# Kernel optimization log

Hardware: AMD Instinct MI355X
Metric: run time of the kernel (lower is better)

The kernel has to match this reference:

```python
import jax, jax.numpy as jnp
import numpy as np

D_MODEL = 2048
D_INNER = 2048
N_QK = 32
N_V = 32
D_STATE = 64
D_CONV = 4
CHUNK = 128
CONV_DIM = D_INNER + 2 * N_QK * D_STATE  # 6144
IN_OUT = 2 * D_INNER + 2 * N_QK * D_STATE + N_V  # 8224


def setup_inputs() -> dict:
    key = jax.random.key(0)
    ks = jax.random.split(key, 6)
    u = jax.random.normal(ks[0], (2, 4096, D_MODEL), dtype=jnp.float32)
    W_in = jax.random.normal(ks[1], (IN_OUT, D_MODEL), dtype=jnp.float32) * 0.02
    conv_w = jax.random.normal(ks[2], (CONV_DIM, D_CONV), dtype=jnp.float32) * 0.2
    conv_b = jax.random.normal(ks[3], (CONV_DIM,), dtype=jnp.float32) * 0.02
    D = jnp.ones((N_V,), dtype=jnp.float32)
    z_bias = jnp.zeros((D_INNER,), dtype=jnp.float32)
    W_out = jax.random.normal(ks[4], (D_MODEL, D_INNER), dtype=jnp.float32) * 0.02
    return {"u": u, "W_in": W_in, "conv_w": conv_w, "conv_b": conv_b,
            "D": D, "z_bias": z_bias, "W_out": W_out}


def causal_depthwise_conv(x, w, b):
    # x: [B, L, C]; w: [C, K]; b: [C]. Torch Conv1d(groups=C, padding=K-1)[..., :L]
    B, L, C = x.shape
    K = w.shape[1]
    xp = jnp.pad(x, ((0, 0), (K - 1, 0), (0, 0)))
    y = b[None, None, :]
    for k in range(K):
        y = y + xp[:, k:k + L, :] * w[None, None, :, k]
    return y


def ssd_chunk_scan(x, dt, B, C, chunk):
    # Mamba2 SSD with A = -1 per head.
    # x: [b,l,h,p], dt: [b,l,h] (positive), B,C: [b,l,h,n]
    b, l, h, p = x.shape
    n = B.shape[-1]
    nc = l // chunk
    x = x.reshape(b, nc, chunk, h, p)
    dt = dt.reshape(b, nc, chunk, h)
    B = B.reshape(b, nc, chunk, h, n)
    C = C.reshape(b, nc, chunk, h, n)
    a = -dt                                  # A * dt
    cum = jnp.cumsum(a, axis=2)              # [b,nc,q,h]
    xdt = x * dt[..., None]                  # dt_t * x_t
    # ---- intra-chunk (causal, decay exp(cum_q - cum_k), q >= k) ----
    CB = jnp.einsum('bcqhn,bckhn->bchqk', C, B)
    cumT = jnp.swapaxes(cum, 2, 3)           # [b,nc,h,q]
    diff = cumT[..., :, None] - cumT[..., None, :]   # [b,nc,h,q,k]
    mask = jnp.tril(jnp.ones((chunk, chunk), dtype=bool))
    decay = jnp.exp(jnp.where(mask, diff, -jnp.inf))
    y_intra = jnp.einsum('bchqk,bckhp->bcqhp', CB * decay, xdt)
    # ---- per-chunk final states ----
    state_decay = jnp.exp(cum[:, :, -1:, :] - cum)   # [b,nc,q,h]
    states = jnp.einsum('bckhn,bckhp->bchpn', B * state_decay[..., None], xdt)
    chunk_decay = jnp.exp(cum[:, :, -1, :])          # [b,nc,h]
    # ---- inter-chunk recurrence ----
    def step(carry, inp):
        st, cd = inp  # st [b,h,p,n], cd [b,h]
        new = carry * cd[:, :, None, None] + st
        return new, carry  # emit the state *entering* this chunk
    init = jnp.zeros((b, h, p, n), dtype=x.dtype)
    _, prev = jax.lax.scan(step, init,
                           (jnp.moveaxis(states, 1, 0), jnp.moveaxis(chunk_decay, 1, 0)))
    prev = jnp.moveaxis(prev, 0, 1)                  # [b,nc,h,p,n]
    y_inter = jnp.einsum('bcqhn,bchpn->bcqhp', C * jnp.exp(cum)[..., None], prev)
    return (y_intra + y_inter).reshape(b, l, h, p)


def reference(u, W_in, conv_w, conv_b, D, z_bias, W_out):
    b, l, _ = u.shape  # l divisible by CHUNK (padded_len == l)
    xBCzA = jnp.einsum('bld,od->blo', u, W_in)
    xBC = xBCzA[..., :CONV_DIM]
    z = xBCzA[..., CONV_DIM:CONV_DIM + D_INNER]
    A_log = xBCzA[..., CONV_DIM + D_INNER:]
    xBC = causal_depthwise_conv(xBC, conv_w, conv_b)  # activation = identity
    x = xBC[..., :D_INNER]
    Bm = xBC[..., D_INNER:D_INNER + N_QK * D_STATE]
    Cm = xBC[..., D_INNER + N_QK * D_STATE:]
    x = x.reshape(b, l, N_V, D_INNER // N_V)
    Bm = Bm.reshape(b, l, N_QK, D_STATE)
    Cm = Cm.reshape(b, l, N_QK, D_STATE)
    dt = jax.nn.softplus(A_log)                       # [b,l,h]
    x_scan = x / dt[..., None]
    y = ssd_chunk_scan(x_scan, dt, Bm, Cm, CHUNK)
    y = y + D[None, None, :, None] * x                # Du uses undivided x
    y = y.reshape(b, l, D_INNER)
    out = jnp.einsum('bli,oi->blo', y * jax.nn.silu(z + z_bias), W_out)
    return out
```

## Files before the change

kernel.cpp:

```cpp
#include <hip/hip_runtime.h>
#include <math.h>

#define D_MODEL  2048
#define D_INNER  2048
#define N_QK     32
#define N_V      32
#define D_STATE  64
#define D_CONV   4
#define CHUNK    128
#define CONV_DIM 6144
#define IN_OUT   8224
#define BATCH    2
#define SEQ      4096
#define M_ROWS   (BATCH*SEQ)
#define NCHUNK   (SEQ/CHUNK)

typedef unsigned short bf16_t;
typedef __attribute__((ext_vector_type(4))) float f32x4;
typedef __attribute__((ext_vector_type(8))) short bf16x8;

#define SWZ64(r,c)  ((((r)*64)  + (c)) ^ (((r)&7)<<3))
#define SWZ128(r,c) ((((r)*128) + (c)) ^ (((r)&7)<<3))

__device__ __forceinline__ float b2f(bf16_t u) {
    union { unsigned int i; float f; } w; w.i = ((unsigned int)u) << 16; return w.f;
}
__device__ __forceinline__ bf16_t f2b(float f) {
    unsigned int x = __float_as_uint(f);
    return (bf16_t)((x + 0x7FFFu + ((x >> 16) & 1u)) >> 16);
}
__device__ __forceinline__ void store4b(bf16_t* dst, float4 v) {
    ushort4 u; u.x = f2b(v.x); u.y = f2b(v.y); u.z = f2b(v.z); u.w = f2b(v.w);
    *reinterpret_cast<ushort4*>(dst) = u;
}

__device__ __forceinline__ void gload_lds16(const bf16_t* g, bf16_t* l) {
    __builtin_amdgcn_global_load_lds((const __attribute__((address_space(1))) void*)g,
                                     (__attribute__((address_space(3))) void*)l,
                                     16, 0, 0);
}

__global__ __launch_bounds__(256) void f2b_kernel(const float* __restrict__ in,
                                                  bf16_t* __restrict__ out, long n)
{
    const long i = ((long)blockIdx.x * 256 + threadIdx.x) * 4;
    if (i < n) {
        float4 v = *reinterpret_cast<const float4*>(in + i);
        ushort4 o;
        o.x = f2b(v.x); o.y = f2b(v.y); o.z = f2b(v.z); o.w = f2b(v.w);
        *reinterpret_cast<ushort4*>(out + i) = o;
    }
}

template<int NTB, int K, bool OBF16>
__global__ __launch_bounds__(512, 2) void gemm256(const bf16_t* __restrict__ A,
                                                  const bf16_t* __restrict__ B,
                                                  void* __restrict__ Cv,
                                                  long ldc)
{
    constexpr int BK = 64;
    constexpr int NT = K / BK;
    __shared__ bf16_t As[2][256 * BK];
    __shared__ bf16_t Bs[2][256 * BK];

    const int nwg = gridDim.x;
    const int bid = blockIdx.x;
    const int wg  = ((nwg & 7) == 0) ? ((bid & 7) * (nwg >> 3) + (bid >> 3)) : bid;
    const int bm = (wg / NTB) * 256;
    const int bn = (wg % NTB) * 256;

    const int tid  = threadIdx.x;
    const int lane = tid & 63;
    const int wv   = tid >> 6;
    const int wr   = wv >> 2, wc = wv & 3;
    const int l15  = lane & 15, l4 = lane >> 4;

    f32x4 acc[8][4];
    #pragma unroll
    for (int i = 0; i < 8; ++i)
        #pragma unroll
        for (int j = 0; j < 4; ++j) acc[i][j] = (f32x4){0.f, 0.f, 0.f, 0.f};

    const bf16_t* Abase = A + (long)bm * K;
    const bf16_t* Bbase = B + (long)bn * K;

    auto stage = [&](int t, int buf) {
        const bf16_t* Ab = Abase + t * BK;
        const bf16_t* Bb = Bbase + t * BK;
        #pragma unroll
        for (int it = 0; it < 4; ++it) {
            const int seg = it * 512 + tid;
            const int row = seg >> 3, c16 = seg & 7;
            const int sc = (c16 ^ (row & 7)) * 8;
            gload_lds16(Ab + (long)row * K + sc, &As[buf][seg * 8]);
            gload_lds16(Bb + (long)row * K + sc, &Bs[buf][seg * 8]);
        }
    };

    stage(0, 0);
    asm volatile("s_waitcnt vmcnt(0)" ::: "memory");
    __builtin_amdgcn_s_barrier();

    for (int t = 0; t < NT; ++t) {
        const int cur = t & 1;
        if (t + 1 < NT) stage(t + 1, cur ^ 1);
        bf16x8 bfr[4], af[4];
        #pragma unroll
        for (int ks = 0; ks < 2; ++ks) {
            #pragma unroll
            for (int ni = 0; ni < 4; ++ni) {
                const int row = wc * 64 + ni * 16 + l15;
                const int ch = (ks * 4 + l4) ^ (row & 7);
                bfr[ni] = *reinterpret_cast<const bf16x8*>(&Bs[cur][row * 64 + ch * 8]);
            }
            #pragma unroll
            for (int qm = 0; qm < 2; ++qm) {
                #pragma unroll
                for (int mi = 0; mi < 4; ++mi) {
                    const int row = wr * 128 + qm * 64 + mi * 16 + l15;
                    const int ch = (ks * 4 + l4) ^ (row & 7);
                    af[mi] = *reinterpret_cast<const bf16x8*>(&As[cur][row * 64 + ch * 8]);
                }
                __builtin_amdgcn_s_setprio(1);
                #pragma unroll
                for (int mi = 0; mi < 4; ++mi)
                    #pragma unroll
                    for (int ni = 0; ni < 4; ++ni)
                        acc[qm * 4 + mi][ni] = __builtin_amdgcn_mfma_f32_16x16x32_bf16(
                            af[mi], bfr[ni], acc[qm * 4 + mi][ni], 0, 0, 0);
                __builtin_amdgcn_s_setprio(0);
                if (ks * 2 + qm < 3) __builtin_amdgcn_s_barrier();
            }
        }
        asm volatile("s_waitcnt vmcnt(0)" ::: "memory");
        __builtin_amdgcn_s_barrier();
    }

    #pragma unroll
    for (int mf = 0; mf < 8; ++mf) {
        const long grow0 = bm + wr * 128 + mf * 16 + l4 * 4;
        #pragma unroll
        for (int ni = 0; ni < 4; ++ni) {
            const int gcol = bn + wc * 64 + ni * 16 + l15;
            #pragma unroll
            for (int j = 0; j < 4; ++j) {
                if (OBF16)
                    ((bf16_t*)Cv)[(grow0 + j) * ldc + gcol] = f2b(acc[mf][ni][j]);
                else
                    ((float*)Cv)[(grow0 + j) * ldc + gcol] = acc[mf][ni][j];
            }
        }
    }
}

template<int N, int K, bool OBF16>
__global__ __launch_bounds__(256) void gemm_mfma(const bf16_t* __restrict__ A,
                                                 const bf16_t* __restrict__ B,
                                                 void* __restrict__ Cv,
                                                 long ldc)
{
    constexpr int BM = 128, BN = 128, BK = 64;
    constexpr int NTB = (N + BN - 1) / BN;
    __shared__ bf16_t As[BM * BK];
    __shared__ bf16_t Bs[BM * BK];

    const int nwg = gridDim.x;
    const int bid = blockIdx.x;
    const int wg  = ((nwg & 7) == 0) ? ((bid & 7) * (nwg >> 3) + (bid >> 3)) : bid;
    const int bm = (wg / NTB) * BM;
    const int bn = (wg % NTB) * BN;

    const int tid  = threadIdx.x;
    const int lane = tid & 63;
    const int wv   = tid >> 6;
    const int wr   = wv >> 1, wc = wv & 1;

    f32x4 acc[4][4];
    #pragma unroll
    for (int i = 0; i < 4; ++i)
        #pragma unroll
        for (int j = 0; j < 4; ++j) acc[i][j] = (f32x4){0.f, 0.f, 0.f, 0.f};

    for (int k0 = 0; k0 < K; k0 += BK) {
        #pragma unroll
        for (int it = 0; it < 4; ++it) {
            const int seg = it * 256 + tid;
            const int row = seg >> 3, c16 = seg & 7;
            gload_lds16(A + (long)(bm + row) * K + k0 + c16 * 8,
                        &As[row * BK + c16 * 8]);
            int brow = bn + row;
            if constexpr (N % BN != 0) brow = min(brow, N - 1);
            gload_lds16(B + (long)brow * K + k0 + c16 * 8,
                        &Bs[row * BK + c16 * 8]);
        }
        __syncthreads();
        #pragma unroll
        for (int kk = 0; kk < 2; ++kk) {
            bf16x8 af[4], bfr[4];
            const int kc = kk * 32 + (lane >> 4) * 8;
            #pragma unroll
            for (int mi = 0; mi < 4; ++mi) {
                const int row = wr * 64 + mi * 16 + (lane & 15);
                af[mi] = *reinterpret_cast<const bf16x8*>(&As[row * BK + kc]);
            }
            #pragma unroll
            for (int ni = 0; ni < 4; ++ni) {
                const int row = wc * 64 + ni * 16 + (lane & 15);
                bfr[ni] = *reinterpret_cast<const bf16x8*>(&Bs[row * BK + kc]);
            }
            #pragma unroll
            for (int mi = 0; mi < 4; ++mi)
                #pragma unroll
                for (int ni = 0; ni < 4; ++ni)
                    acc[mi][ni] = __builtin_amdgcn_mfma_f32_16x16x32_bf16(
                        af[mi], bfr[ni], acc[mi][ni], 0, 0, 0);
        }
        __syncthreads();
    }

    #pragma unroll
    for (int mi = 0; mi < 4; ++mi) {
        const long row0 = bm + wr * 64 + mi * 16 + ((lane >> 4) << 2);
        #pragma unroll
        for (int ni = 0; ni < 4; ++ni) {
            const int col = bn + wc * 64 + ni * 16 + (lane & 15);
            if (N % BN != 0 && col >= N) continue;
            #pragma unroll
            for (int j = 0; j < 4; ++j) {
                if (OBF16)
                    ((bf16_t*)Cv)[(row0 + j) * ldc + col] = f2b(acc[mi][ni][j]);
                else
                    ((float*)Cv)[(row0 + j) * ldc + col] = acc[mi][ni][j];
            }
        }
    }
}

__device__ __forceinline__ float4 conv4v(const bf16_t* __restrict__ xb, long m, int l,
                                         int col, const float* __restrict__ cw,
                                         const float* __restrict__ cbv)
{
    float4 acc = *reinterpret_cast<const float4*>(cbv + col);
    float4 wc0 = *reinterpret_cast<const float4*>(cw + (long)col * 4);
    float4 wc1 = *reinterpret_cast<const float4*>(cw + (long)col * 4 + 4);
    float4 wc2 = *reinterpret_cast<const float4*>(cw + (long)col * 4 + 8);
    float4 wc3 = *reinterpret_cast<const float4*>(cw + (long)col * 4 + 12);
    const float t0[4] = {wc0.x, wc0.y, wc0.z, wc0.w};
    const float t1[4] = {wc1.x, wc1.y, wc1.z, wc1.w};
    const float t2[4] = {wc2.x, wc2.y, wc2.z, wc2.w};
    const float t3[4] = {wc3.x, wc3.y, wc3.z, wc3.w};
    #pragma unroll
    for (int tap = 0; tap < 4; ++tap) {
        if (l - 3 + tap < 0) continue;
        const bf16_t* p = xb + (m - 3 + tap) * (long)IN_OUT + col;
        ushort4 v = *reinterpret_cast<const ushort4*>(p);
        acc.x = fmaf(b2f(v.x), t0[tap], acc.x);
        acc.y = fmaf(b2f(v.y), t1[tap], acc.y);
        acc.z = fmaf(b2f(v.z), t2[tap], acc.z);
        acc.w = fmaf(b2f(v.w), t3[tap], acc.w);
    }
    return acc;
}

__global__ __launch_bounds__(256) void dt_kernel(const bf16_t* __restrict__ xb,
                                                 float* __restrict__ dt)
{
    const int i = blockIdx.x * 256 + threadIdx.x;
    if (i < M_ROWS * N_V) {
        const int m = i >> 5, h = i & 31;
        const float a = b2f(xb[(long)m * IN_OUT + (CONV_DIM + D_INNER) + h]);
        dt[i] = (a > 20.f) ? a : log1pf(expf(a));
    }
}

__global__ __launch_bounds__(256) void ssd_states(const bf16_t* __restrict__ xb,
                                                  const float* __restrict__ dt,
                                                  const float* __restrict__ cw,
                                                  const float* __restrict__ cbv,
                                                  float* __restrict__ states,
                                                  float* __restrict__ cumbuf,
                                                  float* __restrict__ cdecay)
{
    const int h = blockIdx.x, c = blockIdx.y, b = blockIdx.z;
    __shared__ float sB[CHUNK][68];
    __shared__ float sx[CHUNK][68];
    __shared__ float cum[CHUNK];
    const int t = threadIdx.x;
    const long mbase = (long)b * SEQ + (long)c * CHUNK;
    if (t < CHUNK) cum[t] = -dt[(mbase + t) * N_V + h];
    for (int idx = t; idx < CHUNK * 16; idx += 256) {
        const int k = idx >> 4, q4 = (idx & 15) * 4;
        const long m = mbase + k;
        const int l = (int)(m & (SEQ - 1));
        float4 xv = conv4v(xb, m, l, h * 64 + q4, cw, cbv);
        float4 bv = conv4v(xb, m, l, D_INNER + h * 64 + q4, cw, cbv);
        *reinterpret_cast<float4*>(&sx[k][q4]) = xv;
        *reinterpret_cast<float4*>(&sB[k][q4]) = bv;
    }
    __syncthreads();
    if (t == 0) { float s = 0.f; for (int k = 0; k < CHUNK; ++k) { s += cum[k]; cum[k] = s; } }
    __syncthreads();
    const float clast = cum[CHUNK - 1];
    const int p = t >> 2, n0 = (t & 3) * 16;
    float acc[16];
    #pragma unroll
    for (int j = 0; j < 16; ++j) acc[j] = 0.f;
    for (int k = 0; k < CHUNK; ++k) {
        const float sxk = sx[k][p] * __expf(clast - cum[k]);
        #pragma unroll
        for (int j = 0; j < 16; ++j) acc[j] = fmaf(sB[k][n0 + j], sxk, acc[j]);
    }
    const long cb = ((long)b * NCHUNK + c) * N_QK + h;
    const long sbase = (cb * 64 + p) * 64 + n0;
    #pragma unroll
    for (int j = 0; j < 16; ++j) states[sbase + j] = acc[j];
    if (t < CHUNK) cumbuf[cb * CHUNK + t] = cum[t];
    if (t == 0)   cdecay[cb] = __expf(clast);
}

__global__ __launch_bounds__(256) void ssd_scan(float* __restrict__ states,
                                                const float* __restrict__ cdecay)
{
    const int bh = blockIdx.x;
    const int b = bh >> 5, h = bh & 31;
    const int t = threadIdx.x;
    float carry[16];
    #pragma unroll
    for (int j = 0; j < 16; ++j) carry[j] = 0.f;
    for (int c = 0; c < NCHUNK; ++c) {
        const long cb = ((long)b * NCHUNK + c) * N_QK + h;
        const long base = cb * 4096 + (long)t * 16;
        const float cd = cdecay[cb];
        #pragma unroll
        for (int v = 0; v < 4; ++v) {
            float4 st = *reinterpret_cast<const float4*>(&states[base + v * 4]);
            float4 pv = make_float4(carry[v*4], carry[v*4+1], carry[v*4+2], carry[v*4+3]);
            *reinterpret_cast<float4*>(&states[base + v * 4]) = pv;
            carry[v*4]   = fmaf(carry[v*4],   cd, st.x);
            carry[v*4+1] = fmaf(carry[v*4+1], cd, st.y);
            carry[v*4+2] = fmaf(carry[v*4+2], cd, st.z);
            carry[v*4+3] = fmaf(carry[v*4+3], cd, st.w);
        }
    }
}

__global__ __launch_bounds__(256) void ssd_out(const bf16_t* __restrict__ xb,
                                               const float* __restrict__ cumbuf,
                                               const float* __restrict__ prevst,
                                               const float* __restrict__ Dvec,
                                               const float* __restrict__ zbias,
                                               const float* __restrict__ cw,
                                               const float* __restrict__ cbv,
                                               bf16_t* __restrict__ yz)
{
    const int h = blockIdx.x, c = blockIdx.y, b = blockIdx.z;
    __shared__ bf16_t sC[128 * 64];
    __shared__ bf16_t sB[128 * 64];
    __shared__ bf16_t sXQ[128 * 64];
    __shared__ bf16_t sXT[64 * 128];
    __shared__ bf16_t sP[64 * 64];
    __shared__ float  cum[CHUNK];
    const int t = threadIdx.x;
    const long mbase = (long)b * SEQ + (long)c * CHUNK;
    const long cb = ((long)b * NCHUNK + c) * N_QK + h;
    if (t < CHUNK) cum[t] = cumbuf[cb * CHUNK + t];
    for (int idx = t; idx < CHUNK * 16; idx += 256) {
        const int k = idx >> 4, q4 = (idx & 15) * 4;
        const long m = mbase + k;
        const int l = (int)(m & (SEQ - 1));
        float4 xv = conv4v(xb, m, l, h * 64 + q4, cw, cbv);
        float4 bv = conv4v(xb, m, l, D_INNER + h * 64 + q4, cw, cbv);
        float4 cv = conv4v(xb, m, l, 2 * D_INNER + h * 64 + q4, cw, cbv);
        store4b(&sXQ[SWZ64(k, q4)], xv);
        store4b(&sB [SWZ64(k, q4)], bv);
        store4b(&sC [SWZ64(k, q4)], cv);
    }
    for (int idx = t; idx < 64 * 16; idx += 256) {
        const int p = idx >> 4, q4 = (idx & 15) * 4;
        float4 v = *reinterpret_cast<const float4*>(prevst + cb * 4096 + p * 64 + q4);
        store4b(&sP[SWZ64(p, q4)], v);
    }
    __syncthreads();
    {
        const int j = t & 127;
        const int c8b = (t >> 7) * 4;
        #pragma unroll
        for (int it = 0; it < 4; ++it) {
            const int c8 = c8b + it;
            bf16x8 v = *reinterpret_cast<const bf16x8*>(&sXQ[SWZ64(j, c8 * 8)]);
            #pragma unroll
            for (int e = 0; e < 8; ++e) sXT[SWZ128(c8 * 8 + e, j)] = v[e];
        }
    }
    __syncthreads();

    const int lane = t & 63, wv = t >> 6;
    const int w32 = wv * 32, l15 = lane & 15, l4 = lane >> 4;
    bf16_t* sQ = sXQ;

    f32x4 yac[2][4], iac[2][4];
    #pragma unroll
    for (int mi = 0; mi < 2; ++mi)
        #pragma unroll
        for (int np = 0; np < 4; ++np) {
            yac[mi][np] = (f32x4){0.f, 0.f, 0.f, 0.f};
            iac[mi][np] = (f32x4){0.f, 0.f, 0.f, 0.f};
        }

    #pragma unroll
    for (int H = 0; H < 2; ++H) {
        if (H == 1 && wv < 2) break;
        const int j0 = H * 64;
        f32x4 sac[2][4];
        #pragma unroll
        for (int mi = 0; mi < 2; ++mi)
            #pragma unroll
            for (int nj = 0; nj < 4; ++nj) sac[mi][nj] = (f32x4){0.f, 0.f, 0.f, 0.f};
        #pragma unroll
        for (int kk = 0; kk < 2; ++kk) {
            const int kc = kk * 32 + l4 * 8;
            bf16x8 af0 = *reinterpret_cast<const bf16x8*>(&sC[SWZ64(w32 + l15, kc)]);
            bf16x8 af1 = *reinterpret_cast<const bf16x8*>(&sC[SWZ64(w32 + 16 + l15, kc)]);
            #pragma unroll
            for (int nj = 0; nj < 4; ++nj) {
                bf16x8 bfj = *reinterpret_cast<const bf16x8*>(&sB[SWZ64(j0 + nj * 16 + l15, kc)]);
                if (j0 + nj * 16 <= w32 + 15)
                    sac[0][nj] = __builtin_amdgcn_mfma_f32_16x16x32_bf16(af0, bfj, sac[0][nj], 0, 0, 0);
                if (j0 + nj * 16 <= w32 + 31)
                    sac[1][nj] = __builtin_amdgcn_mfma_f32_16x16x32_bf16(af1, bfj, sac[1][nj], 0, 0, 0);
            }
        }
        #pragma unroll
        for (int mi = 0; mi < 2; ++mi) {
            #pragma unroll
            for (int nj = 0; nj < 4; ++nj) {
                const int jcol = nj * 16 + l15;
                const int jg = j0 + jcol;
                #pragma unroll
                for (int jj = 0; jj < 4; ++jj) {
                    const int i = w32 + mi * 16 + l4 * 4 + jj;
                    const float q = (jg <= i) ? __expf(cum[i] - cum[jg]) * sac[mi][nj][jj] : 0.f;
                    sQ[SWZ64(i, jcol)] = f2b(q);
                }
            }
        }
        #pragma unroll
        for (int kk = 0; kk < 2; ++kk) {
            const int kc = kk * 32 + l4 * 8;
            bf16x8 qa0 = *reinterpret_cast<const bf16x8*>(&sQ[SWZ64(w32 + l15, kc)]);
            bf16x8 qa1 = *reinterpret_cast<const bf16x8*>(&sQ[SWZ64(w32 + 16 + l15, kc)]);
            #pragma unroll
            for (int np = 0; np < 4; ++np) {
                bf16x8 xf = *reinterpret_cast<const bf16x8*>(&sXT[SWZ128(np * 16 + l15, j0 + kc)]);
                yac[0][np] = __builtin_amdgcn_mfma_f32_16x16x32_bf16(qa0, xf, yac[0][np], 0, 0, 0);
                yac[1][np] = __builtin_amdgcn_mfma_f32_16x16x32_bf16(qa1, xf, yac[1][np], 0, 0, 0);
            }
        }
    }
    #pragma unroll
    for (int kk = 0; kk < 2; ++kk) {
        const int kc = kk * 32 + l4 * 8;
        bf16x8 cf0 = *reinterpret_cast<const bf16x8*>(&sC[SWZ64(w32 + l15, kc)]);
        bf16x8 cf1 = *reinterpret_cast<const bf16x8*>(&sC[SWZ64(w32 + 16 + l15, kc)]);
        #pragma unroll
        for (int np = 0; np < 4; ++np) {
            bf16x8 pf = *reinterpret_cast<const bf16x8*>(&sP[SWZ64(np * 16 + l15, kc)]);
            iac[0][np] = __builtin_amdgcn_mfma_f32_16x16x32_bf16(cf0, pf, iac[0][np], 0, 0, 0);
            iac[1][np] = __builtin_amdgcn_mfma_f32_16x16x32_bf16(cf1, pf, iac[1][np], 0, 0, 0);
        }
    }
    const float dh = Dvec[h];
    #pragma unroll
    for (int mi = 0; mi < 2; ++mi) {
        #pragma unroll
        for (int jj = 0; jj < 4; ++jj) {
            const int i = w32 + mi * 16 + l4 * 4 + jj;
            const float ei = __expf(cum[i]);
            const long m = mbase + i;
            const bf16_t* zr = xb + m * (long)IN_OUT + CONV_DIM + h * 64;
            bf16_t* orow = yz + m * (long)D_INNER + h * 64;
            #pragma unroll
            for (int np = 0; np < 4; ++np) {
                const int p = np * 16 + l15;
                const float xval = b2f(sXT[SWZ128(p, i)]);
                const float y = yac[mi][np][jj] + ei * iac[mi][np][jj] + dh * xval;
                const float zv = b2f(zr[p]) + zbias[h * 64 + p];
                const float s = zv / (1.f + __expf(-zv));
                orow[p] = f2b(y * s);
            }
        }
    }
}

extern "C" void kernel_launch(void* const* d_in, const int* in_sizes, int n_in,
                              void* d_out, int out_size, void* d_ws, size_t ws_size,
                              hipStream_t stream)
{
    const float* u      = (const float*)d_in[0];
    const float* W_in   = (const float*)d_in[1];
    const float* conv_w = (const float*)d_in[2];
    const float* conv_b = (const float*)d_in[3];
    const float* Dv     = (const float*)d_in[4];
    const float* z_bias = (const float*)d_in[5];
    const float* W_out  = (const float*)d_in[6];
    float* out = (float*)d_out;

    char* w = (char*)d_ws;
    bf16_t* xbcza = (bf16_t*)w;  w += (long)M_ROWS * IN_OUT * 2;
    bf16_t* wob   = (bf16_t*)w;  w += (long)2048 * 2048 * 2;
    char* ureg = w;
    bf16_t* ub  = (bf16_t*)ureg;
    bf16_t* wib = (bf16_t*)(ureg + (long)M_ROWS * D_MODEL * 2);
    bf16_t* yzb = (bf16_t*)ureg;
    float*  dtb = (float*)(ureg + (long)M_ROWS * D_INNER * 2);
    float*  cumb   = dtb + (long)M_ROWS * N_V;
    float*  states = cumb + (long)BATCH * NCHUNK * N_QK * CHUNK;
    float*  cdec   = states + (long)BATCH * NCHUNK * N_QK * 4096;

    f2b_kernel<<<(int)(((long)M_ROWS * D_MODEL / 4 + 255) / 256), 256, 0, stream>>>(
        u, ub, (long)M_ROWS * D_MODEL);
    f2b_kernel<<<(int)(((long)IN_OUT * D_MODEL / 4 + 255) / 256), 256, 0, stream>>>(
        W_in, wib, (long)IN_OUT * D_MODEL);
    f2b_kernel<<<(int)(((long)D_MODEL * D_INNER / 4 + 255) / 256), 256, 0, stream>>>(
        W_out, wob, (long)D_MODEL * D_INNER);

    gemm256<32, D_MODEL, true><<<(M_ROWS / 256) * 32, 512, 0, stream>>>(
        ub, wib, xbcza, IN_OUT);
    gemm_mfma<32, D_MODEL, true><<<(M_ROWS / 128), 256, 0, stream>>>(
        ub, wib + (long)8192 * D_MODEL, xbcza + 8192, IN_OUT);

    dt_kernel<<<(M_ROWS * N_V + 255) / 256, 256, 0, stream>>>(xbcza, dtb);

    ssd_states<<<dim3(N_QK, NCHUNK, BATCH), 256, 0, stream>>>(xbcza, dtb, conv_w, conv_b,
                                                              states, cumb, cdec);

    ssd_scan<<<BATCH * N_QK, 256, 0, stream>>>(states, cdec);

    ssd_out<<<dim3(N_QK, NCHUNK, BATCH), 256, 0, stream>>>(xbcza, cumb, states, Dv, z_bias,
                                                           conv_w, conv_b, yzb);

    gemm256<8, D_INNER, false><<<(M_ROWS / 256) * 8, 512, 0, stream>>>(
        yzb, wob, out, D_MODEL);
}
```

Before: 867.6 us.

## Use 4-stage LDS pipeline with BK=32 and partial vmcnt waits in GEMM

Halves the K-tile to 32 and moves from double buffering to a four-buffer ring that prefetches three tiles ahead. The main loop now waits with partial vmcnt counts instead of draining all outstanding loads every iteration. The LDS layout changes to pack two 32-wide rows per 64-element swizzled line. The goal is to hide global-load latency better. In exchange there are twice as many loop iterations and barriers per K, and the vmcnt accounting has to stay exact for correctness.

New measurement: 931.2 us. 1.07x slower.

```diff
diff --git a/kernel.cpp b/kernel.cpp
--- a/kernel.cpp
+++ b/kernel.cpp
@@ -58,10 +58,10 @@
                                                   void* __restrict__ Cv,
                                                   long ldc)
 {
-    constexpr int BK = 64;
+    constexpr int BK = 32;
     constexpr int NT = K / BK;
-    __shared__ bf16_t As[2][256 * BK];
-    __shared__ bf16_t Bs[2][256 * BK];
+    __shared__ bf16_t As[4][128 * 64];
+    __shared__ bf16_t Bs[4][128 * 64];
 
     const int nwg = gridDim.x;
     const int bid = blockIdx.x;
@@ -88,51 +88,61 @@
         const bf16_t* Ab = Abase + t * BK;
         const bf16_t* Bb = Bbase + t * BK;
         #pragma unroll
-        for (int it = 0; it < 4; ++it) {
-            const int seg = it * 512 + tid;
-            const int row = seg >> 3, c16 = seg & 7;
-            const int sc = (c16 ^ (row & 7)) * 8;
-            gload_lds16(Ab + (long)row * K + sc, &As[buf][seg * 8]);
-            gload_lds16(Bb + (long)row * K + sc, &Bs[buf][seg * 8]);
+        for (int it = 0; it < 2; ++it) {
+            const int s = it * 512 + tid;
+            const int pair = s >> 3, c16 = s & 7;
+            const int lc  = c16 ^ (pair & 7);
+            const int row = 2 * pair + (lc >> 2);
+            const long go = (long)row * K + (lc & 3) * 8;
+            gload_lds16(Ab + go, &As[buf][s * 8]);
+            gload_lds16(Bb + go, &Bs[buf][s * 8]);
         }
     };
-
-    stage(0, 0);
-    asm volatile("s_waitcnt vmcnt(0)" ::: "memory");
+    auto rdA = [&](int buf, int r) {
+        const int pair = r >> 1;
+        const int lc = ((r & 1) << 2) | l4;
+        return *reinterpret_cast<const bf16x8*>(&As[buf][pair * 64 + ((lc ^ (pair & 7)) << 3)]);
+    };
+    auto rdB = [&](int buf, int r) {
+        const int pair = r >> 1;
+        const int lc = ((r & 1) << 2) | l4;
+        return *reinterpret_cast<const bf16x8*>(&Bs[buf][pair * 64 + ((lc ^ (pair & 7)) << 3)]);
+    };
+
+    stage(0, 0); stage(1, 1); stage(2, 2);
+    asm volatile("s_waitcnt vmcnt(8)" ::: "memory");
     __builtin_amdgcn_s_barrier();
 
     for (int t = 0; t < NT; ++t) {
-        const int cur = t & 1;
-        if (t + 1 < NT) stage(t + 1, cur ^ 1);
+        const int buf = t & 3;
+        if (t + 3 < NT) stage(t + 3, (t + 3) & 3);
         bf16x8 bfr[4], af[4];
         #pragma unroll
-        for (int ks = 0; ks < 2; ++ks) {
-            #pragma unroll
-            for (int ni = 0; ni < 4; ++ni) {
-                const int row = wc * 64 + ni * 16 + l15;
-                const int ch = (ks * 4 + l4) ^ (row & 7);
-                bfr[ni] = *reinterpret_cast<const bf16x8*>(&Bs[cur][row * 64 + ch * 8]);
-            }
-            #pragma unroll
-            for (int qm = 0; qm < 2; ++qm) {
-                #pragma unroll
-                for (int mi = 0; mi < 4; ++mi) {
-                    const int row = wr * 128 + qm * 64 + mi * 16 + l15;
-                    const int ch = (ks * 4 + l4) ^ (row & 7);
-                    af[mi] = *reinterpret_cast<const bf16x8*>(&As[cur][row * 64 + ch * 8]);
-                }
-                __builtin_amdgcn_s_setprio(1);
-                #pragma unroll
-                for (int mi = 0; mi < 4; ++mi)
-                    #pragma unroll
-                    for (int ni = 0; ni < 4; ++ni)
-                        acc[qm * 4 + mi][ni] = __builtin_amdgcn_mfma_f32_16x16x32_bf16(
-                            af[mi], bfr[ni], acc[qm * 4 + mi][ni], 0, 0, 0);
-                __builtin_amdgcn_s_setprio(0);
-                if (ks * 2 + qm < 3) __builtin_amdgcn_s_barrier();
-            }
-        }
-        asm volatile("s_waitcnt vmcnt(0)" ::: "memory");
+        for (int ni = 0; ni < 4; ++ni) bfr[ni] = rdB(buf, wc * 64 + ni * 16 + l15);
+        #pragma unroll
+        for (int mi = 0; mi < 4; ++mi) af[mi] = rdA(buf, wr * 128 + mi * 16 + l15);
+        __builtin_amdgcn_s_setprio(1);
+        #pragma unroll
+        for (int mi = 0; mi < 4; ++mi)
+            #pragma unroll
+            for (int ni = 0; ni < 4; ++ni)
+                acc[mi][ni] = __builtin_amdgcn_mfma_f32_16x16x32_bf16(
+                    af[mi], bfr[ni], acc[mi][ni], 0, 0, 0);
+        __builtin_amdgcn_s_setprio(0);
+        __builtin_amdgcn_s_barrier();
+        #pragma unroll
+        for (int mi = 0; mi < 4; ++mi) af[mi] = rdA(buf, wr * 128 + 64 + mi * 16 + l15);
+        __builtin_amdgcn_s_setprio(1);
+        #pragma unroll
+        for (int mi = 0; mi < 4; ++mi)
+            #pragma unroll
+            for (int ni = 0; ni < 4; ++ni)
+                acc[4 + mi][ni] = __builtin_amdgcn_mfma_f32_16x16x32_bf16(
+                    af[mi], bfr[ni], acc[4 + mi][ni], 0, 0, 0);
+        __builtin_amdgcn_s_setprio(0);
+        if (t < NT - 3)       { asm volatile("s_waitcnt vmcnt(8)" ::: "memory"); }
+        else if (t == NT - 3) { asm volatile("s_waitcnt vmcnt(4)" ::: "memory"); }
+        else if (t == NT - 2) { asm volatile("s_waitcnt vmcnt(0)" ::: "memory"); }
         __builtin_amdgcn_s_barrier();
     }
 
```
